# Optimization experiments

Hardware: AMD Instinct MI355X
Metric: run time of the kernel (lower is better)

The kernel has to match this reference:

```python
import jax, jax.numpy as jnp
import numpy as np

B, S, H = 8, 2048, 1024


def setup_inputs() -> dict:
    key = jax.random.key(0)
    ks = jax.random.split(key, 12)
    s = 1.0 / np.sqrt(H)
    return {
        "_q": jax.random.normal(ks[0], (B, S, H), jnp.float32),
        "_kv": jax.random.normal(ks[1], (B, S, H), jnp.float32),
        "W_kv": jax.random.normal(ks[2], (H, 2 * H), jnp.float32) * s,
        "b_kv": jnp.zeros((2 * H,), jnp.float32),
        "W_q": jax.random.normal(ks[3], (H, H), jnp.float32) * s,
        "b_q": jnp.zeros((H,), jnp.float32),
        "W1": jax.random.normal(ks[4], (H, 4 * H), jnp.float32) * s,
        "b1": jnp.zeros((4 * H,), jnp.float32),
        "W2": jax.random.normal(ks[5], (4 * H, H), jnp.float32) * (1.0 / np.sqrt(4 * H)),
        "b2": jnp.zeros((H,), jnp.float32),
    }


def reference(_q, _kv, W_kv, b_kv, W_q, b_q, W1, b1, W2, b2):
    # kv projection then split into k, v: [B,S,H] each
    kv = _kv @ W_kv + b_kv
    k, v = jnp.split(kv, 2, axis=-1)
    q = _q @ W_q + b_q
    # NOTE: original module does single-head attention with NO 1/sqrt(d) scale
    scores = jnp.einsum('bqh,bkh->bqk', q, k)          # [B,Sq,Sk]
    attn = jax.nn.softmax(scores, axis=-1)
    out = jnp.einsum('bqk,bkh->bqh', attn, v)          # [B,Sq,H]
    # MLP: Linear -> exact GELU -> (Dropout=identity in eval) -> Linear
    hidden = jax.nn.gelu(out @ W1 + b1, approximate=False)
    return hidden @ W2 + b2
```

## Files before the change

### kernel.cpp

```cpp
#include <hip/hip_runtime.h>
#include <hip/hip_bf16.h>

typedef __attribute__((ext_vector_type(8))) short short8;
typedef __attribute__((ext_vector_type(8))) _Float16 half8;
typedef __attribute__((ext_vector_type(4))) _Float16 half4v;
typedef __attribute__((ext_vector_type(4))) float f32x4;
typedef unsigned short us;

#define GLDS16(G, L) __builtin_amdgcn_global_load_lds( \
    (const __attribute__((address_space(1))) void*)(G), \
    (__attribute__((address_space(3))) void*)(L), 16, 0, 0)

__global__ void k_sentinel(float* p) {
    if (threadIdx.x == 0 && blockIdx.x == 0) p[0] = 12345.0f;
}

__device__ __forceinline__ float fast_gelu(float x) {
    float ax = fabsf(x) * 0.70710678118654752f;
    float t = __frcp_rn(fmaf(0.3275911f, ax, 1.0f));
    float p = fmaf(1.061405429f, t, -1.453152027f);
    p = fmaf(p, t, 1.421413741f);
    p = fmaf(p, t, -0.284496736f);
    p = fmaf(p, t, 0.254829592f);
    p = p * t * __expf(-ax * ax);
    float erfv = __builtin_copysignf(1.0f - p, x);
    return 0.5f * x * (1.0f + erfv);
}

__global__ void k_cast(const float* __restrict__ in, _Float16* __restrict__ out, long n4) {
    long i = (long)blockIdx.x * blockDim.x + threadIdx.x;
    long stride = (long)gridDim.x * blockDim.x;
    for (; i < n4; i += stride) {
        float4 v = ((const float4*)in)[i];
        half4v h;
        h[0] = (_Float16)v.x; h[1] = (_Float16)v.y;
        h[2] = (_Float16)v.z; h[3] = (_Float16)v.w;
        ((half4v*)out)[i] = h;
    }
}

__global__ void k_wtransh(const float* __restrict__ in, _Float16* __restrict__ out,
                          int K, int N) {
    __shared__ float tile[32][33];
    int n0 = blockIdx.x * 32, k0 = blockIdx.y * 32;
    int tx = threadIdx.x, ty = threadIdx.y;
#pragma unroll
    for (int r = ty; r < 32; r += 8)
        tile[r][tx] = in[(size_t)(k0 + r) * N + n0 + tx];
    __syncthreads();
#pragma unroll
    for (int r = ty; r < 32; r += 8)
        out[(size_t)(n0 + r) * K + k0 + tx] = (_Float16)tile[tx][r];
}

__device__ __forceinline__ float wredmax(float v) {
#pragma unroll
    for (int off = 32; off > 0; off >>= 1) v = fmaxf(v, __shfl_xor(v, off, 64));
    return v;
}
__device__ __forceinline__ float wredsum(float v) {
#pragma unroll
    for (int off = 32; off > 0; off >>= 1) v += __shfl_xor(v, off, 64);
    return v;
}

__global__ __launch_bounds__(256) void k_softmax(const float* __restrict__ S,
                                                 _Float16* __restrict__ P) {
    __shared__ float red[8];
    size_t base = (size_t)blockIdx.x * 2048;
    int t = threadIdx.x;
    float4 a = ((const float4*)(S + base))[2 * t];
    float4 b = ((const float4*)(S + base))[2 * t + 1];
    float v[8] = {a.x, a.y, a.z, a.w, b.x, b.y, b.z, b.w};
    float m = v[0];
#pragma unroll
    for (int j = 1; j < 8; j++) m = fmaxf(m, v[j]);
    m = wredmax(m);
    int wv = t >> 6;
    if ((t & 63) == 0) red[wv] = m;
    __syncthreads();
    m = fmaxf(fmaxf(red[0], red[1]), fmaxf(red[2], red[3]));
    float s = 0.f;
#pragma unroll
    for (int j = 0; j < 8; j++) { v[j] = __expf(v[j] - m); s += v[j]; }
    s = wredsum(s);
    if ((t & 63) == 0) red[4 + wv] = s;
    __syncthreads();
    s = red[4] + red[5] + red[6] + red[7];
    float inv = 1.f / s;
    half4v o0, o1;
#pragma unroll
    for (int j = 0; j < 4; j++) o0[j] = (_Float16)(v[j] * inv);
#pragma unroll
    for (int j = 0; j < 4; j++) o1[j] = (_Float16)(v[4 + j] * inv);
    ((half4v*)(P + base))[2 * t] = o0;
    ((half4v*)(P + base))[2 * t + 1] = o1;
}

template <int OUT_MODE, bool GELU_ACT>
__global__ __launch_bounds__(256, 2) void k_gemm64(
    const us* __restrict__ A, const us* __restrict__ B,
    const float* __restrict__ bias, void* __restrict__ C,
    int N, int K, long sA, long sB, long sC) {
    __shared__ __align__(16) us ldsA[8192];
    __shared__ __align__(16) us ldsB[8192];

    const int tid = threadIdx.x;
    const int wave = tid >> 6, lane = tid & 63;
    const int wr = wave >> 1, wc = wave & 1;
    const int l15 = lane & 15, l4 = lane >> 4;
    const int m0 = blockIdx.x * 128, n0 = blockIdx.y * 128;

    const us* pA = A + (size_t)blockIdx.z * sA;
    const us* pB = B + (size_t)blockIdx.z * sB;
    const size_t zC = (size_t)blockIdx.z * sC;

    f32x4 acc[4][4] = {};

    auto stage = [&](const us* __restrict__ g, us* l, int r0, int kk) {
#pragma unroll
        for (int i = 0; i < 4; i++) {
            int s = (i << 8) + tid;
            int row = s >> 3;
            int cl = (s & 7) ^ (row & 7);
            const us* src = g + (size_t)(r0 + row) * K + kk + (cl << 3);
            us* dst = l + (((i << 8) + (wave << 6)) << 3);
            GLDS16(src, dst);
        }
    };

    for (int kk = 0; kk < K; kk += 64) {
        stage(pA, ldsA, m0, kk);
        stage(pB, ldsB, n0, kk);
        __syncthreads();

#pragma unroll
        for (int ks = 0; ks < 2; ks++) {
            short8 af[4], bf[4];
#pragma unroll
            for (int f = 0; f < 4; f++) {
                int ra = (wr << 6) + (f << 4) + l15;
                af[f] = *(const short8*)(
                    &ldsA[(ra << 6) + ((((ks << 2) | l4) ^ (ra & 7)) << 3)]);
                int rb = (wc << 6) + (f << 4) + l15;
                bf[f] = *(const short8*)(
                    &ldsB[(rb << 6) + ((((ks << 2) | l4) ^ (rb & 7)) << 3)]);
            }
#pragma unroll
            for (int fm = 0; fm < 4; fm++)
#pragma unroll
                for (int fn = 0; fn < 4; fn++)
                    acc[fm][fn] = __builtin_amdgcn_mfma_f32_16x16x32_f16(
                        __builtin_bit_cast(half8, af[fm]), __builtin_bit_cast(half8, bf[fn]),
                        acc[fm][fn], 0, 0, 0);
        }
        __syncthreads();
    }

    float bv[4];
#pragma unroll
    for (int fn = 0; fn < 4; fn++)
        bv[fn] = bias ? bias[n0 + (wc << 6) + (fn << 4) + l15] : 0.f;

#pragma unroll
    for (int fm = 0; fm < 4; fm++) {
        int rbase = m0 + (wr << 6) + (fm << 4) + (l4 << 2);
#pragma unroll
        for (int fn = 0; fn < 4; fn++) {
            int col = n0 + (wc << 6) + (fn << 4) + l15;
#pragma unroll
            for (int r = 0; r < 4; r++) {
                float x = acc[fm][fn][r] + bv[fn];
                if (GELU_ACT) x = fast_gelu(x);
                size_t row = (size_t)(rbase + r);
                if (OUT_MODE == 5) {
                    size_t o = ((row >> 11) * (size_t)N + (size_t)col) * 2048 + (row & 2047);
                    ((_Float16*)C)[o] = (_Float16)x;
                } else {
                    size_t o = zC + row * N + col;
                    if (OUT_MODE == 0) ((float*)C)[o] = x;
                    else               ((_Float16*)C)[o] = (_Float16)x;
                }
            }
        }
    }
}

extern "C" void kernel_launch(void* const* d_in, const int* in_sizes, int n_in,
                              void* d_out, int out_size, void* d_ws, size_t ws_size,
                              hipStream_t stream) {
    (void)in_sizes; (void)n_in; (void)out_size;
    const float* g_q   = (const float*)d_in[0];
    const float* g_kv  = (const float*)d_in[1];
    const float* g_Wkv = (const float*)d_in[2];
    const float* g_bkv = (const float*)d_in[3];
    const float* g_Wq  = (const float*)d_in[4];
    const float* g_bq  = (const float*)d_in[5];
    const float* g_W1  = (const float*)d_in[6];
    const float* g_b1  = (const float*)d_in[7];
    const float* g_W2  = (const float*)d_in[8];
    const float* g_b2  = (const float*)d_in[9];

    const size_t MiB = 1048576ull;
    const long SH = 2048L * 1024;
    const long SS = 2048L * 2048;
    char* ws = (char*)d_ws;
    dim3 tb32(32, 8);

    if (ws_size < 176 * MiB) {
        k_sentinel<<<1, 64, 0, stream>>>((float*)d_out);
        return;
    }

    _Float16* xq  = (_Float16*)ws;
    char*     REGION = ws + 32 * MiB;
    _Float16* kf    = (_Float16*)REGION;
    _Float16* vT    = (_Float16*)(REGION + 32 * MiB);
    _Float16* P_all = (_Float16*)(REGION + 64 * MiB);
    _Float16* hidden = (_Float16*)REGION;
    char* wreg = ws + 160 * MiB;
    _Float16* WkvT = (_Float16*)wreg;
    _Float16* WqT  = (_Float16*)(wreg + 4 * MiB);
    _Float16* W1T  = (_Float16*)wreg;
    _Float16* W2T  = (_Float16*)(wreg + 8 * MiB);

    _Float16* xkv      = (_Float16*)d_out;
    float*    scores_c = (float*)d_out;
    _Float16* q_all    = (_Float16*)((char*)d_out + 32 * MiB);

    k_wtransh<<<dim3(64, 32), tb32, 0, stream>>>(g_Wkv, WkvT, 1024, 2048);
    k_wtransh<<<dim3(32, 32), tb32, 0, stream>>>(g_Wq, WqT, 1024, 1024);
    k_cast<<<4096, 256, 0, stream>>>(g_kv, xkv, 4194304);
    k_cast<<<4096, 256, 0, stream>>>(g_q, xq, 4194304);

    k_gemm64<4, false><<<dim3(128, 8, 1), 256, 0, stream>>>(
        (const us*)xkv, (const us*)WkvT, g_bkv, kf, 1024, 1024, 0, 0, 0);
    k_gemm64<5, false><<<dim3(128, 8, 1), 256, 0, stream>>>(
        (const us*)xkv, (const us*)(WkvT + (size_t)1024 * 1024), g_bkv + 1024, vT,
        1024, 1024, 0, 0, 0);
    k_gemm64<4, false><<<dim3(128, 8, 1), 256, 0, stream>>>(
        (const us*)xq, (const us*)WqT, g_bq, q_all, 1024, 1024, 0, 0, 0);

    for (int c = 0; c < 4; ++c) {
        size_t ro = (size_t)c * 4096 * 1024;
        k_gemm64<0, false><<<dim3(16, 16, 2), 256, 0, stream>>>(
            (const us*)(q_all + ro), (const us*)(kf + ro), nullptr, scores_c,
            2048, 1024, SH, SH, SS);
        k_softmax<<<4096, 256, 0, stream>>>(scores_c, P_all + (size_t)c * 2 * SS);
    }

    k_gemm64<4, false><<<dim3(16, 8, 8), 256, 0, stream>>>(
        (const us*)P_all, (const us*)vT, nullptr, xq, 1024, 2048, SS, SH, SH);

    k_wtransh<<<dim3(128, 32), tb32, 0, stream>>>(g_W1, W1T, 1024, 4096);
    k_wtransh<<<dim3(32, 128), tb32, 0, stream>>>(g_W2, W2T, 4096, 1024);
    k_gemm64<4, true><<<dim3(128, 32, 1), 256, 0, stream>>>(
        (const us*)xq, (const us*)W1T, g_b1, hidden, 4096, 1024, 0, 0, 0);
    k_gemm64<0, false><<<dim3(128, 8, 1), 256, 0, stream>>>(
        (const us*)hidden, (const us*)W2T, g_b2, d_out, 1024, 4096, 0, 0, 0);
}
```

Measured before the change: 714.3 us.

## Add double-buffered LDS GEMM kernel for the MLP projections

```diff
diff --git a/kernel.cpp b/kernel.cpp
--- a/kernel.cpp
+++ b/kernel.cpp
@@ -181,6 +181,104 @@
                     if (OUT_MODE == 0) ((float*)C)[o] = x;
                     else               ((_Float16*)C)[o] = (_Float16)x;
                 }
+            }
+        }
+    }
+}
+
+template <int OUT_MODE, bool GELU_ACT>
+__global__ __launch_bounds__(256, 2) void k_gemmdb(
+    const us* __restrict__ A, const us* __restrict__ B,
+    const float* __restrict__ bias, void* __restrict__ C,
+    int N, int K, long sA, long sB, long sC) {
+    __shared__ __align__(16) us lds[2][2][8192];
+
+    const int tid = threadIdx.x;
+    const int wave = tid >> 6, lane = tid & 63;
+    const int wr = wave >> 1, wc = wave & 1;
+    const int l15 = lane & 15, l4 = lane >> 4;
+    const int m0 = blockIdx.x * 128, n0 = blockIdx.y * 128;
+
+    const us* pA = A + (size_t)blockIdx.z * sA;
+    const us* pB = B + (size_t)blockIdx.z * sB;
+    const size_t zC = (size_t)blockIdx.z * sC;
+
+    f32x4 acc[4][4] = {};
+
+    auto stage = [&](const us* __restrict__ g, us* l, int r0, int kk) {
+#pragma unroll
+        for (int i = 0; i < 4; i++) {
+            int s = (i << 8) + tid;
+            int row = s >> 3;
+            int cl = (s & 7) ^ (row & 7);
+            const us* src = g + (size_t)(r0 + row) * K + kk + (cl << 3);
+            us* dst = l + (((i << 8) + (wave << 6)) << 3);
+            GLDS16(src, dst);
+        }
+    };
+
+    stage(pA, &lds[0][0][0], m0, 0);
+    stage(pB, &lds[0][1][0], n0, 0);
+
+    const int NT = K >> 6;
+    for (int t = 0; t < NT; ++t) {
+        const int cur = t & 1;
+        if (t + 1 < NT) {
+            stage(pA, &lds[cur ^ 1][0][0], m0, (t + 1) << 6);
+            stage(pB, &lds[cur ^ 1][1][0], n0, (t + 1) << 6);
+            __builtin_amdgcn_sched_barrier(0);
+            asm volatile("s_waitcnt vmcnt(8)" ::: "memory");
+        } else {
+            asm volatile("s_waitcnt vmcnt(0)" ::: "memory");
+        }
+        __builtin_amdgcn_s_barrier();
+        __builtin_amdgcn_sched_barrier(0);
+
+        const us* la = &lds[cur][0][0];
+        const us* lb = &lds[cur][1][0];
+#pragma unroll
+        for (int ks = 0; ks < 2; ks++) {
+            short8 af[4], bf[4];
+#pragma unroll
+            for (int f = 0; f < 4; f++) {
+                int ra = (wr << 6) + (f << 4) + l15;
+                af[f] = *(const short8*)(&la[(ra << 6) + ((((ks << 2) | l4) ^ (ra & 7)) << 3)]);
+                int rb = (wc << 6) + (f << 4) + l15;
+                bf[f] = *(const short8*)(&lb[(rb << 6) + ((((ks << 2) | l4) ^ (rb & 7)) << 3)]);
+            }
+            __builtin_amdgcn_s_setprio(1);
+#pragma unroll
+            for (int fm = 0; fm < 4; fm++)
+#pragma unroll
+                for (int fn = 0; fn < 4; fn++)
+                    acc[fm][fn] = __builtin_amdgcn_mfma_f32_16x16x32_f16(
+                        __builtin_bit_cast(half8, af[fm]), __builtin_bit_cast(half8, bf[fn]),
+                        acc[fm][fn], 0, 0, 0);
+            __builtin_amdgcn_s_setprio(0);
+        }
+        __builtin_amdgcn_sched_barrier(0);
+        __builtin_amdgcn_s_barrier();
+    }
+
+    float bv[4];
+#pragma unroll
+    for (int fn = 0; fn < 4; fn++)
+        bv[fn] = bias ? bias[n0 + (wc << 6) + (fn << 4) + l15] : 0.f;
+
+#pragma unroll
+    for (int fm = 0; fm < 4; fm++) {
+        int rbase = m0 + (wr << 6) + (fm << 4) + (l4 << 2);
+#pragma unroll
+        for (int fn = 0; fn < 4; fn++) {
+            int col = n0 + (wc << 6) + (fn << 4) + l15;
+#pragma unroll
+            for (int r = 0; r < 4; r++) {
+                float x = acc[fm][fn][r] + bv[fn];
+                if (GELU_ACT) x = fast_gelu(x);
+                size_t row = (size_t)(rbase + r);
+                size_t o = zC + row * N + col;
+                if (OUT_MODE == 0) ((float*)C)[o] = x;
+                else               ((_Float16*)C)[o] = (_Float16)x;
             }
         }
     }
@@ -254,8 +352,8 @@
 
     k_wtransh<<<dim3(128, 32), tb32, 0, stream>>>(g_W1, W1T, 1024, 4096);
     k_wtransh<<<dim3(32, 128), tb32, 0, stream>>>(g_W2, W2T, 4096, 1024);
-    k_gemm64<4, true><<<dim3(128, 32, 1), 256, 0, stream>>>(
+    k_gemmdb<4, true><<<dim3(128, 32, 1), 256, 0, stream>>>(
         (const us*)xq, (const us*)W1T, g_b1, hidden, 4096, 1024, 0, 0, 0);
-    k_gemm64<0, false><<<dim3(128, 8, 1), 256, 0, stream>>>(
+    k_gemmdb<0, false><<<dim3(128, 8, 1), 256, 0, stream>>>(
         (const us*)hidden, (const us*)W2T, g_b2, d_out, 1024, 4096, 0, 0, 0);
 }
```

New measurement: 733.9 us. +2.7%, slower.
